# Optimization experiments

Hardware: AMD Instinct MI355X
Metric: run time of the kernel (lower is better)

The kernel has to match this reference:

```python
import jax, jax.numpy as jnp
import numpy as np

B, N, E = 16, 512, 6144          # graphs, sites/graph, edges/graph
D = 256                          # embed_dimension
RBF_DIM = 128
M = 6                            # num_messages
MAXZ = 84                        # max_atomic_num
INIT_MAX_DIST, INIT_GAP = 7.0, 30.0


def setup_inputs() -> dict:
    key = jax.random.key(0)
    ks = jax.random.split(key, 20)
    s = 0.02
    inp = {
        "site_class": jax.random.randint(ks[0], (B, N), 0, MAXZ, dtype=jnp.int64),
        "distance": jax.random.uniform(ks[1], (B, E), dtype=jnp.float32) * INIT_MAX_DIST,
        "connectivity": jax.random.randint(ks[2], (B, E, 2), 0, N, dtype=jnp.int64),
        # learned parameters
        "atom_emb": jax.random.normal(ks[3], (MAXZ, D), jnp.float32) * s,
        "mean_emb": jnp.zeros((MAXZ, 1), jnp.float32),  # Constant(output_bias=0.0)
        "centers": jnp.arange(RBF_DIM, dtype=jnp.float32) * (INIT_MAX_DIST / RBF_DIM),
        "gap": jnp.float32(INIT_GAP),
        "bond_W": jax.random.normal(ks[4], (RBF_DIM, D), jnp.float32) * s,
        "bond_b": jnp.zeros((D,), jnp.float32),
        "offset_W": jax.random.normal(ks[5], (D, 1), jnp.float32) * 1e-6,
        "offset_b": jnp.zeros((1,), jnp.float32),
        # per-message EdgeUpdate ConcatDense: Dense(2D, relu) -> Dense(D), input 3D
        "edge_W1": jax.random.normal(ks[6], (M, 3 * D, 2 * D), jnp.float32) * s,
        "edge_b1": jnp.zeros((M, 2 * D), jnp.float32),
        "edge_W2": jax.random.normal(ks[7], (M, 2 * D, D), jnp.float32) * s,
        "edge_b2": jnp.zeros((M, D), jnp.float32),
        # per-message NodeUpdate ConcatDense: input 2D
        "node_W1": jax.random.normal(ks[8], (M, 2 * D, 2 * D), jnp.float32) * s,
        "node_b1": jnp.zeros((M, 2 * D), jnp.float32),
        "node_W2": jax.random.normal(ks[9], (M, 2 * D, D), jnp.float32) * s,
        "node_b2": jnp.zeros((M, D), jnp.float32),
    }
    return inp


def _gather(x, idx):
    # x: [B, N, D], idx: [B, E] -> [B, E, D]
    return x[jnp.arange(x.shape[0])[:, None], idx]


def reference(site_class, distance, connectivity,
              atom_emb, mean_emb, centers, gap, bond_W, bond_b,
              offset_W, offset_b,
              edge_W1, edge_b1, edge_W2, edge_b2,
              node_W1, node_b1, node_W2, node_b2):
    atom_mask = site_class != 0                     # [B, N] (Embedding mask_zero)
    bond_mask = distance != 0.0                     # [B, E] (RBFExpansion mask)

    atom_state = atom_emb[site_class]               # [B, N, D]
    atom_mean = mean_emb[site_class]                # [B, N, 1]

    # RBF expansion: exp(-gap * (d - centers)^2), masked distances -> 1.0
    d = distance[..., None]
    d = jnp.where(d != 0.0, d, 1.0)
    rbf = jnp.exp(-((d - centers) ** 2) * gap)      # [B, E, RBF_DIM]
    bond_state = rbf @ bond_W + bond_b              # [B, E, D]

    bidx = jnp.arange(site_class.shape[0])[:, None]
    idx0 = connectivity[..., 0]                     # scatter target
    idx1 = connectivity[..., 1]                     # message source

    n_msg = edge_W1.shape[0]
    for i in range(n_msg):
        # EdgeUpdate: concat(bond, src_atom, tgt_atom) -> Dense(2D, relu) -> Dense(D)
        src = _gather(atom_state, idx1)
        tgt = _gather(atom_state, idx0)
        h = jnp.concatenate([bond_state, src, tgt], axis=-1)      # [B, E, 3D]
        h = jax.nn.relu(h @ edge_W1[i] + edge_b1[i])
        h = h @ edge_W2[i] + edge_b2[i]
        h = jnp.where(bond_mask[..., None], h, 0.0)
        bond_state = bond_state + h

        # NodeUpdate: concat(src_atom, bond) -> MLP -> segment-sum onto idx0
        src = _gather(atom_state, idx1)
        m = jnp.concatenate([src, bond_state], axis=-1)           # [B, E, 2D]
        m = jax.nn.relu(m @ node_W1[i] + node_b1[i])
        m = m @ node_W2[i] + node_b2[i]
        new_atom = jnp.zeros_like(atom_state).at[bidx, idx0].add(m)
        new_atom = jnp.where(atom_mask[..., None], new_atom, 0.0)
        atom_state = atom_state + new_atom

    atom_mean = atom_mean + (atom_state @ offset_W + offset_b)   # [B, N, 1]

    # masked global average pooling over sites
    mask_f = atom_mask[..., None].astype(atom_mean.dtype)
    pooled = jnp.sum(atom_mean * mask_f, axis=1) / jnp.sum(mask_f, axis=1)
    return pooled  # [B, 1]
```

## Files before the change

### kernel.cpp

```cpp
#include <hip/hip_runtime.h>
#include <hip/hip_bf16.h>
#include <stdint.h>
#include <stddef.h>

#define Bb 16
#define Nn 512
#define Ee 6144
#define Dd 256
#define ROWS (Bb * Ee)
#define HALF (ROWS / 2)

typedef short bf16x8 __attribute__((ext_vector_type(8)));
typedef float f32x4 __attribute__((ext_vector_type(4)));

__device__ __forceinline__ unsigned short f2bf(float f) {
  union { float f; unsigned u; } v; v.f = f;
  return (unsigned short)((v.u + 0x7fffu + ((v.u >> 16) & 1u)) >> 16);
}

__device__ __forceinline__ void gload16(const void* g, void* l) {
  __builtin_amdgcn_global_load_lds(
      (const __attribute__((address_space(1))) void*)g,
      (__attribute__((address_space(3))) void*)l, 16, 0, 0);
}

__global__ void transpose_w(const float* __restrict__ in, unsigned short* __restrict__ out,
                            int K, int Ncol) {
  __shared__ float tile[32][33];
  const float* inb = in + (size_t)blockIdx.z * K * Ncol;
  unsigned short* outb = out + (size_t)blockIdx.z * K * Ncol;
  int bk = blockIdx.x * 32, bn = blockIdx.y * 32;
  int tx = threadIdx.x, ty = threadIdx.y;
#pragma unroll
  for (int i = 0; i < 32; i += 8)
    tile[ty + i][tx] = inb[(size_t)(bk + ty + i) * Ncol + (bn + tx)];
  __syncthreads();
#pragma unroll
  for (int i = 0; i < 32; i += 8)
    outb[(size_t)(bn + ty + i) * K + (bk + tx)] = f2bf(tile[tx][ty + i]);
}

__global__ void atom_init(const int* __restrict__ cls, const float* __restrict__ emb,
                          float* __restrict__ atom, unsigned short* __restrict__ atomBf) {
  int s_ = blockIdx.x, d = threadIdx.x;
  size_t o = (size_t)s_ * Dd + d;
  float v = emb[(size_t)cls[s_] * Dd + d];
  atom[o] = v;
  atomBf[o] = f2bf(v);
}

__global__ void atom_fix(const int* __restrict__ cls, const float* __restrict__ emb,
                         float* __restrict__ atom, unsigned short* __restrict__ atomBf) {
  int s_ = blockIdx.x, d = threadIdx.x;
  size_t o = (size_t)s_ * Dd + d;
  float v = (cls[s_] == 0) ? emb[d] : atom[o];
  atom[o] = v;
  atomBf[o] = f2bf(v);
}

__global__ __launch_bounds__(256, 2) void gemm_rbf(
    const unsigned short* __restrict__ Wt, const float* __restrict__ bias,
    const float* __restrict__ dist, const float* __restrict__ centers,
    const float* __restrict__ gapP, float* __restrict__ bond,
    unsigned short* __restrict__ bondBf) {
  __shared__ __align__(16) unsigned short lA[128 * 64];
  __shared__ __align__(16) unsigned short lB[128 * 64];
  const int t = threadIdx.x;
  const int bm = blockIdx.x * 128, bn = blockIdx.y * 128;
  const int srow = t & 127, skc = (t >> 7) * 32;
  const int m = bm + srow;
  float dval = dist[m]; if (dval == 0.f) dval = 1.f;
  float gapv = *gapP;
  const unsigned short* pBt = Wt + (size_t)(bn + srow) * 128 + skc;
  const int wid = t >> 6, lane = t & 63;
  const int wm = (wid & 1) * 64, wn = (wid >> 1) * 64;
  const int fr = lane & 15, fk0 = (lane >> 4) * 8;
  f32x4 acc[4][4] = {};
  for (int k0 = 0; k0 < 128; k0 += 64) {
    union __align__(16) { unsigned short us[32]; bf16x8 v[4]; } ab, bb;
#pragma unroll
    for (int j = 0; j < 32; j++) {
      float x = dval - centers[k0 + skc + j];
      ab.us[j] = f2bf(__expf(-gapv * x * x));
    }
    const bf16x8* s = (const bf16x8*)(pBt + k0);
#pragma unroll
    for (int c = 0; c < 4; c++) bb.v[c] = s[c];
    __syncthreads();
#pragma unroll
    for (int c = 0; c < 4; c++) {
      int byteo = (skc + c * 8) * 2;
      int swz = byteo ^ ((srow & 7) << 4);
      *(bf16x8*)((char*)lA + srow * 128 + swz) = ab.v[c];
      *(bf16x8*)((char*)lB + srow * 128 + swz) = bb.v[c];
    }
    __syncthreads();
#pragma unroll
    for (int kk = 0; kk < 64; kk += 32) {
      bf16x8 af[4], bfq[4];
#pragma unroll
      for (int f = 0; f < 4; f++) {
        int r = wm + f * 16 + fr;
        af[f] = *(const bf16x8*)((const char*)lA + r * 128 + (((kk + fk0) * 2) ^ ((r & 7) << 4)));
        int cq = wn + f * 16 + fr;
        bfq[f] = *(const bf16x8*)((const char*)lB + cq * 128 + (((kk + fk0) * 2) ^ ((cq & 7) << 4)));
      }
#pragma unroll
      for (int i = 0; i < 4; i++)
#pragma unroll
        for (int j = 0; j < 4; j++)
          acc[i][j] = __builtin_amdgcn_mfma_f32_16x16x32_bf16(af[i], bfq[j], acc[i][j], 0, 0, 0);
    }
  }
#pragma unroll
  for (int i = 0; i < 4; i++)
#pragma unroll
    for (int j = 0; j < 4; j++) {
      int gcol = bn + wn + j * 16 + fr;
      float bvv = bias[gcol];
#pragma unroll
      for (int v = 0; v < 4; v++) {
        int grow = bm + wm + i * 16 + (lane >> 4) * 4 + v;
        float val = acc[i][j][v] + bvv;
        size_t o = (size_t)grow * Dd + gcol;
        bond[o] = val;
        bondBf[o] = f2bf(val);
      }
    }
}

struct GP {
  const unsigned short* Wt;
  const float* bias;
  const unsigned short* bondBf;
  const unsigned short* atomBf;
  const unsigned short* h1;
  const int* conn;
  const float* dist;
  float* bond;
  unsigned short* outH1;
  unsigned short* outBondBf;
  float* atomMaster;
  int rowBase;
};

#define A_EDGE1 0
#define A_NODE1 1
#define A_H1    2
#define EP_H1RELU 0
#define EP_EDGE2  1
#define EP_NODE2  2

template <int K, int NC, int AL, int EP>
__global__ __launch_bounds__(512, 4) void gemm128(GP p) {
  __shared__ __align__(16) char lds[65536];
  constexpr int BOFF = 32768;
  const int t = threadIdx.x;
  const int w = t >> 6, l = t & 63;
  constexpr int NT = NC / 128;

  const int nwg = gridDim.x;
  const int q8 = nwg >> 3;
  const int sb = (blockIdx.x & 7) * q8 + (blockIdx.x >> 3);
  const int bn = (sb % NT) * 128;
  const int bm = (sb / NT) * 128;

  const char* pA0[2]; const char* pA1[2]; const char* pA2[2]; const char* pB[2];
#pragma unroll
  for (int i = 0; i < 2; i++) {
    int r = (w * 2 + i) * 8 + (l >> 3);
    int swz = (((l & 7) ^ (r & 7)) << 4);
    if (AL == A_H1) {
      pA0[i] = (const char*)p.h1 + (size_t)(bm + r) * (K * 2) + swz;
      pA1[i] = pA0[i]; pA2[i] = pA0[i];
    } else {
      int gr = p.rowBase + bm + r;
      int b = gr / Ee;
      int i0 = p.conn[2 * gr], i1 = p.conn[2 * gr + 1];
      const char* bondRow = (const char*)p.bondBf + (size_t)gr * 512 + swz;
      const char* srcRow  = (const char*)p.atomBf + ((size_t)b * Nn + i1) * 512 + swz;
      const char* tgtRow  = (const char*)p.atomBf + ((size_t)b * Nn + i0) * 512 + swz;
      if (AL == A_EDGE1) { pA0[i] = bondRow; pA1[i] = srcRow; pA2[i] = tgtRow; }
      else               { pA0[i] = srcRow;  pA1[i] = bondRow; pA2[i] = bondRow; }
    }
    pB[i] = (const char*)p.Wt + (size_t)(bn + r) * (K * 2) + swz;
  }

  const int fr = l & 15;
  const int q4 = l >> 4;
  const int wm = (w >> 2) * 64;
  const int wn = (w & 3) * 32;

  f32x4 acc[4][2] = {};

  auto stage = [&](int pb, int k0) {
#pragma unroll
    for (int i = 0; i < 2; i++) {
      const char* src;
      if (AL == A_H1)         src = pA0[i] + k0 * 2;
      else if (AL == A_EDGE1) { int s = k0 >> 8; src = (s == 0 ? pA0[i] : (s == 1 ? pA1[i] : pA2[i])) + (k0 & 255) * 2; }
      else                    src = (k0 < 256 ? pA0[i] : pA1[i]) + (k0 & 255) * 2;
      gload16(src, lds + pb * 16384 + (w * 2 + i) * 1024);
      gload16(pB[i] + k0 * 2, lds + BOFF + pb * 16384 + (w * 2 + i) * 1024);
    }
  };

  auto compute = [&](int pb) {
#pragma unroll
    for (int kk = 0; kk < 2; kk++) {
      const int ck = kk * 4 + q4;
      bf16x8 av[4], bv[2];
#pragma unroll
      for (int f = 0; f < 4; f++) {
        int r = wm + f * 16 + fr;
        av[f] = *(const bf16x8*)(lds + pb * 16384 + r * 128 + ((ck ^ (r & 7)) << 4));
      }
#pragma unroll
      for (int n = 0; n < 2; n++) {
        int rq = wn + n * 16 + fr;
        bv[n] = *(const bf16x8*)(lds + BOFF + pb * 16384 + rq * 128 + ((ck ^ (rq & 7)) << 4));
      }
#pragma unroll
      for (int f = 0; f < 4; f++)
#pragma unroll
        for (int n = 0; n < 2; n++)
          acc[f][n] = __builtin_amdgcn_mfma_f32_16x16x32_bf16(av[f], bv[n], acc[f][n], 0, 0, 0);
    }
  };

  constexpr int nT = K / 64;
  stage(0, 0);
  __syncthreads();
  for (int tt = 0; tt < nT; tt++) {
    int pb = tt & 1;
    if (tt + 1 < nT) stage(pb ^ 1, (tt + 1) * 64);
    compute(pb);
    __syncthreads();
  }

  float bias2[2];
#pragma unroll
  for (int n = 0; n < 2; n++) bias2[n] = p.bias[bn + wn + n * 16 + fr];

#pragma unroll
  for (int f = 0; f < 4; f++) {
#pragma unroll
    for (int v = 0; v < 4; v++) {
      int lrow = bm + wm + f * 16 + q4 * 4 + v;
      if (EP == EP_H1RELU) {
#pragma unroll
        for (int n = 0; n < 2; n++) {
          int gcol = bn + wn + n * 16 + fr;
          float val = acc[f][n][v] + bias2[n];
          p.outH1[(size_t)lrow * 512 + gcol] = f2bf(fmaxf(val, 0.f));
        }
      } else if (EP == EP_EDGE2) {
        int grow = p.rowBase + lrow;
        if (p.dist[grow] != 0.f) {
#pragma unroll
          for (int n = 0; n < 2; n++) {
            int gcol = bn + wn + n * 16 + fr;
            size_t o = (size_t)grow * Dd + gcol;
            float nv = p.bond[o] + acc[f][n][v] + bias2[n];
            p.bond[o] = nv;
            p.outBondBf[o] = f2bf(nv);
          }
        }
      } else {
        int grow = p.rowBase + lrow;
        int b = grow / Ee;
        int tg = p.conn[2 * grow];
        float* dst = p.atomMaster + ((size_t)b * Nn + tg) * Dd;
#pragma unroll
        for (int n = 0; n < 2; n++) {
          int gcol = bn + wn + n * 16 + fr;
          atomicAdd(dst + gcol, acc[f][n][v] + bias2[n]);
        }
      }
    }
  }
}

__global__ void pool_k(const float* __restrict__ atom, const int* __restrict__ cls,
                       const float* __restrict__ meanEmb, const float* __restrict__ oW,
                       const float* __restrict__ ob, float* __restrict__ out) {
  __shared__ float w[Dd];
  __shared__ float red[256];
  __shared__ float redc[256];
  int b = blockIdx.x, t = threadIdx.x;
  w[t] = oW[t];
  __syncthreads();
  float sum = 0.f, cnt = 0.f;
  for (int n = t; n < Nn; n += 256) {
    int site = b * Nn + n;
    int c = cls[site];
    const float* a = atom + (size_t)site * Dd;
    float dot = 0.f;
    for (int d = 0; d < Dd; d++) dot += a[d] * w[d];
    if (c != 0) { sum += meanEmb[c] + dot + ob[0]; cnt += 1.f; }
  }
  red[t] = sum; redc[t] = cnt;
  __syncthreads();
  for (int s = 128; s > 0; s >>= 1) {
    if (t < s) { red[t] += red[t + s]; redc[t] += redc[t + s]; }
    __syncthreads();
  }
  if (t == 0) out[b] = red[0] / redc[0];
}

extern "C" void kernel_launch(void* const* d_in, const int* in_sizes, int n_in,
                              void* d_out, int out_size, void* d_ws, size_t ws_size,
                              hipStream_t stream) {
  const int* site_class = (const int*)d_in[0];
  const float* distance = (const float*)d_in[1];
  const int* conn       = (const int*)d_in[2];
  const float* atom_emb = (const float*)d_in[3];
  const float* mean_emb = (const float*)d_in[4];
  const float* centers  = (const float*)d_in[5];
  const float* gapP     = (const float*)d_in[6];
  const float* bond_W   = (const float*)d_in[7];
  const float* bond_b   = (const float*)d_in[8];
  const float* offset_W = (const float*)d_in[9];
  const float* offset_b = (const float*)d_in[10];
  const float* edge_W1  = (const float*)d_in[11];
  const float* edge_b1  = (const float*)d_in[12];
  const float* edge_W2  = (const float*)d_in[13];
  const float* edge_b2  = (const float*)d_in[14];
  const float* node_W1  = (const float*)d_in[15];
  const float* node_b1  = (const float*)d_in[16];
  const float* node_W2  = (const float*)d_in[17];
  const float* node_b2  = (const float*)d_in[18];

  char* ws = (char*)d_ws;
  float* atom            = (float*)(ws + 0);
  unsigned short* atomBf = (unsigned short*)(ws + 8388608);
  float* bond            = (float*)(ws + 12582912);
  unsigned short* bondBf = (unsigned short*)(ws + 113246208);
  unsigned short* h1     = (unsigned short*)(ws + 163577856);
  unsigned short* bWT    = (unsigned short*)(ws + 213909504);
  unsigned short* eW1T   = (unsigned short*)(ws + 213975040);
  unsigned short* eW2T   = (unsigned short*)(ws + 218693632);
  unsigned short* nW1T   = (unsigned short*)(ws + 220266496);
  unsigned short* nW2T   = (unsigned short*)(ws + 223412224);

  dim3 tb(32, 8);
  transpose_w<<<dim3(4, 8, 1), tb, 0, stream>>>(bond_W, bWT, 128, 256);
  transpose_w<<<dim3(24, 16, 6), tb, 0, stream>>>(edge_W1, eW1T, 768, 512);
  transpose_w<<<dim3(16, 8, 6), tb, 0, stream>>>(edge_W2, eW2T, 512, 256);
  transpose_w<<<dim3(16, 16, 6), tb, 0, stream>>>(node_W1, nW1T, 512, 512);
  transpose_w<<<dim3(16, 8, 6), tb, 0, stream>>>(node_W2, nW2T, 512, 256);

  atom_init<<<Bb * Nn, 256, 0, stream>>>(site_class, atom_emb, atom, atomBf);
  gemm_rbf<<<dim3(768, 2), 256, 0, stream>>>(bWT, bond_b, distance, centers, gapP, bond, bondBf);

  GP base{};
  base.conn = conn; base.dist = distance;
  base.bondBf = bondBf; base.atomBf = atomBf; base.h1 = h1;
  base.bond = bond; base.outH1 = h1; base.outBondBf = bondBf; base.atomMaster = atom;

  for (int i = 0; i < 6; i++) {
    for (int h = 0; h < 2; h++) {
      GP q = base; q.rowBase = h * HALF;
      q.Wt = eW1T + (size_t)i * 512 * 768; q.bias = edge_b1 + i * 512;
      gemm128<768, 512, A_EDGE1, EP_H1RELU><<<1536, 512, 0, stream>>>(q);
      GP q2 = base; q2.rowBase = h * HALF;
      q2.Wt = eW2T + (size_t)i * 256 * 512; q2.bias = edge_b2 + i * 256;
      gemm128<512, 256, A_H1, EP_EDGE2><<<768, 512, 0, stream>>>(q2);
    }
    for (int h = 0; h < 2; h++) {
      GP q = base; q.rowBase = h * HALF;
      q.Wt = nW1T + (size_t)i * 512 * 512; q.bias = node_b1 + i * 512;
      gemm128<512, 512, A_NODE1, EP_H1RELU><<<1536, 512, 0, stream>>>(q);
      GP q2 = base; q2.rowBase = h * HALF;
      q2.Wt = nW2T + (size_t)i * 256 * 512; q2.bias = node_b2 + i * 256;
      gemm128<512, 256, A_H1, EP_NODE2><<<768, 512, 0, stream>>>(q2);
    }
    atom_fix<<<Bb * Nn, 256, 0, stream>>>(site_class, atom_emb, atom, atomBf);
  }

  pool_k<<<Bb, 256, 0, stream>>>(atom, site_class, mean_emb, offset_W, offset_b, (float*)d_out);
}
```

Measured before the change: 2.102 ms.

## Store bond state as bf16 hi/lo pair and process all rows per launch

Replaces the fp32 bond master plus bf16 copy with a bf16 high part and a bf16 residual low part. The GEMM A operand reads the high half directly, and the edge epilogue rebuilds fp32 from hi+lo, which cuts the bond footprint from 6 to 4 bytes per element. The h1 buffer is now large enough to hold all rows, so the two half-batch launches per GEMM merge into a single launch with twice the grid. This trades a little precision and some extra conversion ALU work for less memory traffic and fewer launches.

```diff
diff --git a/kernel.cpp b/kernel.cpp
--- a/kernel.cpp
+++ b/kernel.cpp
@@ -8,7 +8,6 @@
 #define Ee 6144
 #define Dd 256
 #define ROWS (Bb * Ee)
-#define HALF (ROWS / 2)
 
 typedef short bf16x8 __attribute__((ext_vector_type(8)));
 typedef float f32x4 __attribute__((ext_vector_type(4)));
@@ -16,6 +15,10 @@
 __device__ __forceinline__ unsigned short f2bf(float f) {
   union { float f; unsigned u; } v; v.f = f;
   return (unsigned short)((v.u + 0x7fffu + ((v.u >> 16) & 1u)) >> 16);
+}
+__device__ __forceinline__ float bf2f(unsigned short h) {
+  union { unsigned u; float f; } v; v.u = ((unsigned)h) << 16;
+  return v.f;
 }
 
 __device__ __forceinline__ void gload16(const void* g, void* l) {
@@ -61,8 +64,8 @@
 __global__ __launch_bounds__(256, 2) void gemm_rbf(
     const unsigned short* __restrict__ Wt, const float* __restrict__ bias,
     const float* __restrict__ dist, const float* __restrict__ centers,
-    const float* __restrict__ gapP, float* __restrict__ bond,
-    unsigned short* __restrict__ bondBf) {
+    const float* __restrict__ gapP, unsigned short* __restrict__ bondHi,
+    unsigned short* __restrict__ bondLo) {
   __shared__ __align__(16) unsigned short lA[128 * 64];
   __shared__ __align__(16) unsigned short lB[128 * 64];
   const int t = threadIdx.x;
@@ -123,8 +126,9 @@
         int grow = bm + wm + i * 16 + (lane >> 4) * 4 + v;
         float val = acc[i][j][v] + bvv;
         size_t o = (size_t)grow * Dd + gcol;
-        bond[o] = val;
-        bondBf[o] = f2bf(val);
+        unsigned short hi = f2bf(val);
+        bondHi[o] = hi;
+        bondLo[o] = f2bf(val - bf2f(hi));
       }
     }
 }
@@ -132,16 +136,15 @@
 struct GP {
   const unsigned short* Wt;
   const float* bias;
-  const unsigned short* bondBf;
+  const unsigned short* bondHi;
+  unsigned short* bondLo;
   const unsigned short* atomBf;
   const unsigned short* h1;
   const int* conn;
   const float* dist;
-  float* bond;
   unsigned short* outH1;
-  unsigned short* outBondBf;
+  unsigned short* outBondHi;
   float* atomMaster;
-  int rowBase;
 };
 
 #define A_EDGE1 0
@@ -174,10 +177,10 @@
       pA0[i] = (const char*)p.h1 + (size_t)(bm + r) * (K * 2) + swz;
       pA1[i] = pA0[i]; pA2[i] = pA0[i];
     } else {
-      int gr = p.rowBase + bm + r;
+      int gr = bm + r;
       int b = gr / Ee;
       int i0 = p.conn[2 * gr], i1 = p.conn[2 * gr + 1];
-      const char* bondRow = (const char*)p.bondBf + (size_t)gr * 512 + swz;
+      const char* bondRow = (const char*)p.bondHi + (size_t)gr * 512 + swz;
       const char* srcRow  = (const char*)p.atomBf + ((size_t)b * Nn + i1) * 512 + swz;
       const char* tgtRow  = (const char*)p.atomBf + ((size_t)b * Nn + i0) * 512 + swz;
       if (AL == A_EDGE1) { pA0[i] = bondRow; pA1[i] = srcRow; pA2[i] = tgtRow; }
@@ -246,28 +249,28 @@
   for (int f = 0; f < 4; f++) {
 #pragma unroll
     for (int v = 0; v < 4; v++) {
-      int lrow = bm + wm + f * 16 + q4 * 4 + v;
+      int grow = bm + wm + f * 16 + q4 * 4 + v;
       if (EP == EP_H1RELU) {
 #pragma unroll
         for (int n = 0; n < 2; n++) {
           int gcol = bn + wn + n * 16 + fr;
           float val = acc[f][n][v] + bias2[n];
-          p.outH1[(size_t)lrow * 512 + gcol] = f2bf(fmaxf(val, 0.f));
+          p.outH1[(size_t)grow * 512 + gcol] = f2bf(fmaxf(val, 0.f));
         }
       } else if (EP == EP_EDGE2) {
-        int grow = p.rowBase + lrow;
         if (p.dist[grow] != 0.f) {
 #pragma unroll
           for (int n = 0; n < 2; n++) {
             int gcol = bn + wn + n * 16 + fr;
             size_t o = (size_t)grow * Dd + gcol;
-            float nv = p.bond[o] + acc[f][n][v] + bias2[n];
-            p.bond[o] = nv;
-            p.outBondBf[o] = f2bf(nv);
+            float cur = bf2f(p.bondHi[o]) + bf2f(p.bondLo[o]);
+            float nv = cur + acc[f][n][v] + bias2[n];
+            unsigned short hi = f2bf(nv);
+            p.outBondHi[o] = hi;
+            p.bondLo[o] = f2bf(nv - bf2f(hi));
           }
         }
       } else {
-        int grow = p.rowBase + lrow;
         int b = grow / Ee;
         int tg = p.conn[2 * grow];
         float* dst = p.atomMaster + ((size_t)b * Nn + tg) * Dd;
@@ -334,9 +337,9 @@
   char* ws = (char*)d_ws;
   float* atom            = (float*)(ws + 0);
   unsigned short* atomBf = (unsigned short*)(ws + 8388608);
-  float* bond            = (float*)(ws + 12582912);
-  unsigned short* bondBf = (unsigned short*)(ws + 113246208);
-  unsigned short* h1     = (unsigned short*)(ws + 163577856);
+  unsigned short* bondHi = (unsigned short*)(ws + 12582912);
+  unsigned short* bondLo = (unsigned short*)(ws + 62914560);
+  unsigned short* h1     = (unsigned short*)(ws + 113246208);
   unsigned short* bWT    = (unsigned short*)(ws + 213909504);
   unsigned short* eW1T   = (unsigned short*)(ws + 213975040);
   unsigned short* eW2T   = (unsigned short*)(ws + 218693632);
@@ -351,29 +354,33 @@
   transpose_w<<<dim3(16, 8, 6), tb, 0, stream>>>(node_W2, nW2T, 512, 256);
 
   atom_init<<<Bb * Nn, 256, 0, stream>>>(site_class, atom_emb, atom, atomBf);
-  gemm_rbf<<<dim3(768, 2), 256, 0, stream>>>(bWT, bond_b, distance, centers, gapP, bond, bondBf);
+  gemm_rbf<<<dim3(768, 2), 256, 0, stream>>>(bWT, bond_b, distance, centers, gapP, bondHi, bondLo);
 
   GP base{};
   base.conn = conn; base.dist = distance;
-  base.bondBf = bondBf; base.atomBf = atomBf; base.h1 = h1;
-  base.bond = bond; base.outH1 = h1; base.outBondBf = bondBf; base.atomMaster = atom;
+  base.bondHi = bondHi; base.bondLo = bondLo; base.atomBf = atomBf; base.h1 = h1;
+  base.outH1 = h1; base.outBondHi = bondHi; base.atomMaster = atom;
 
   for (int i = 0; i < 6; i++) {
-    for (int h = 0; h < 2; h++) {
-      GP q = base; q.rowBase = h * HALF;
+    {
+      GP q = base;
       q.Wt = eW1T + (size_t)i * 512 * 768; q.bias = edge_b1 + i * 512;
-      gemm128<768, 512, A_EDGE1, EP_H1RELU><<<1536, 512, 0, stream>>>(q);
-      GP q2 = base; q2.rowBase = h * HALF;
-      q2.Wt = eW2T + (size_t)i * 256 * 512; q2.bias = edge_b2 + i * 256;
-      gemm128<512, 256, A_H1, EP_EDGE2><<<768, 512, 0, stream>>>(q2);
-    }
-    for (int h = 0; h < 2; h++) {
-      GP q = base; q.rowBase = h * HALF;
+      gemm128<768, 512, A_EDGE1, EP_H1RELU><<<3072, 512, 0, stream>>>(q);
+    }
+    {
+      GP q = base;
+      q.Wt = eW2T + (size_t)i * 256 * 512; q.bias = edge_b2 + i * 256;
+      gemm128<512, 256, A_H1, EP_EDGE2><<<1536, 512, 0, stream>>>(q);
+    }
+    {
+      GP q = base;
       q.Wt = nW1T + (size_t)i * 512 * 512; q.bias = node_b1 + i * 512;
-      gemm128<512, 512, A_NODE1, EP_H1RELU><<<1536, 512, 0, stream>>>(q);
-      GP q2 = base; q2.rowBase = h * HALF;
-      q2.Wt = nW2T + (size_t)i * 256 * 512; q2.bias = node_b2 + i * 256;
-      gemm128<512, 256, A_H1, EP_NODE2><<<768, 512, 0, stream>>>(q2);
+      gemm128<512, 512, A_NODE1, EP_H1RELU><<<3072, 512, 0, stream>>>(q);
+    }
+    {
+      GP q = base;
+      q.Wt = nW2T + (size_t)i * 256 * 512; q.bias = node_b2 + i * 256;
+      gemm128<512, 256, A_H1, EP_NODE2><<<1536, 512, 0, stream>>>(q);
     }
     atom_fix<<<Bb * Nn, 256, 0, stream>>>(site_class, atom_emb, atom, atomBf);
   }
```

Measured after the change: 1.953 ms, median of 4. 7.1% less time.
